# Kernel tuning notes

Measured on AMD Instinct MI355X. Metric: run time of the kernel, lower is better.

The kernel has to match this reference:

```python
import jax, jax.numpy as jnp
import numpy as np

PERIOD = 7   # statsmodels seasonal_decompose period used in season()
L_P = 16     # patch length hardcoded in patches()
STRIDE = 8   # stride hardcoded in patches()

B, C, L, D = 16, 64, 512, 768


def _decompose(x):
    """Vectorized additive seasonal_decompose (period=7) over last axis.

    Matches statsmodels: trend = centered 7-pt moving average (edges NaN in
    statsmodels; represented as 0 here so the math stays finite), seasonal =
    de-meaned per-phase average of the detrended interior, resid = x - trend
    - seasonal on the valid interior (0 at edges, where statsmodels has NaN).
    x: [B, C, L]
    """
    Lx = x.shape[-1]
    half = PERIOD // 2  # 3
    cs = jnp.concatenate([jnp.zeros(x.shape[:-1] + (1,), x.dtype), jnp.cumsum(x, -1)], -1)
    ma = (cs[..., PERIOD:] - cs[..., :-PERIOD]) / PERIOD  # [B,C,L-6] centers 3..L-4
    trend = jnp.zeros_like(x).at[..., half:Lx - half].set(ma)
    idx = jnp.arange(Lx)
    mask = (idx >= half) & (idx < Lx - half)          # valid interior
    ph = idx % PERIOD
    det = jnp.where(mask, x - trend, 0.0)             # detrended (0 where invalid)
    Pm = jax.nn.one_hot(ph, PERIOD, dtype=x.dtype) * mask[:, None].astype(x.dtype)  # [L,7]
    sums = jnp.einsum('bcl,lp->bcp', det, Pm)         # per-phase sums over valid idx
    counts = Pm.sum(0)                                # per-phase valid counts
    pavg = sums / counts
    pavg = pavg - pavg.mean(-1, keepdims=True)        # de-mean the 7 phase averages
    seasonal = jnp.take(pavg, ph, axis=-1)            # tile to [B,C,L]
    resid = jnp.where(mask, x - trend - seasonal, 0.0)
    return trend, seasonal, resid


def setup_inputs() -> dict:
    key = jax.random.key(0)
    ks = jax.random.split(key, 12)
    s = 0.02
    return {
        'data_x': jax.random.normal(ks[0], (B, C, L), jnp.float32),
        'data_y': jax.random.normal(ks[1], (B, C, L), jnp.float32),
        'gamma': jax.random.uniform(ks[2], (B, C, L), jnp.float32),
        'beta': jax.random.uniform(ks[3], (B, C, L), jnp.float32),
        'w_trend': jax.random.normal(ks[4], (L_P, L), jnp.float32) * s,
        'b_trend': jax.random.normal(ks[5], (L_P,), jnp.float32) * s,
        'w_seasonal': jax.random.normal(ks[6], (L_P, L), jnp.float32) * s,
        'b_seasonal': jax.random.normal(ks[7], (L_P,), jnp.float32) * s,
        'w_resid': jax.random.normal(ks[8], (L_P, L), jnp.float32) * s,
        'b_resid': jax.random.normal(ks[9], (L_P,), jnp.float32) * s,
        'w_g': jax.random.normal(ks[10], (D, 3 * L_P), jnp.float32) * s,
        'b_g': jax.random.normal(ks[11], (D,), jnp.float32) * s,
    }


def reference(data_x, data_y, gamma, beta, w_trend, b_trend, w_seasonal,
              b_seasonal, w_resid, b_resid, w_g, b_g):
    Lx = data_x.shape[-1]
    # transformed(): RevIN-like affine with mean/sqrt(var) (epsi=0, unbiased var)
    mean = data_x.mean(1)
    var = data_x.var(1, ddof=1)
    m = (mean / jnp.sqrt(var))[:, None, :]
    xt = gamma * (data_x - m) + beta
    # season() detaches its input in the original
    xt = jax.lax.stop_gradient(xt)
    trend, seasonal, resid = _decompose(xt)
    # patches(): per-stream Linear(L->16), concat, Linear(48->D)
    t = trend @ w_trend.T + b_trend          # [B,C,16]
    s = seasonal @ w_seasonal.T + b_seasonal
    r = resid @ w_resid.T + b_resid
    cat = jnp.concatenate([t, s, r], -1)     # [B,C,48]
    p = cat @ w_g.T + b_g                    # [B,C,D]
    # unsqueeze(2).expand(...) before cat -> every patch slot is identical
    N_p = int((Lx + L_P) / STRIDE + 2)
    return jnp.broadcast_to(p[:, :, None, :], p.shape[:2] + (N_p, p.shape[-1]))
```

## Files before the change

### kernel.cpp

```cpp
#include <hip/hip_runtime.h>

#define Bx 16
#define Cx 64
#define Lx 512
#define Dx 768
#define NPx 68
#define PER 7

__global__ void mean_var_kernel(const float* __restrict__ x,
                                float* __restrict__ m) {
    int idx = blockIdx.x * blockDim.x + threadIdx.x;
    if (idx >= Bx * Lx) return;
    int b = idx / Lx, l = idx - b * Lx;
    const float* xp = x + (size_t)b * Cx * Lx + l;
    float s = 0.f, ss = 0.f;
#pragma unroll 8
    for (int c = 0; c < Cx; ++c) {
        float v = xp[(size_t)c * Lx];
        s += v;
        ss += v * v;
    }
    float mean = s / (float)Cx;
    float var = (ss - s * s / (float)Cx) / (float)(Cx - 1);
    m[idx] = mean * rsqrtf(var);
}

__global__ __launch_bounds__(256) void token_kernel(
    const float* __restrict__ x, const float* __restrict__ gamma,
    const float* __restrict__ beta, const float* __restrict__ m,
    const float* __restrict__ w_t, const float* __restrict__ b_t,
    const float* __restrict__ w_s, const float* __restrict__ b_s,
    const float* __restrict__ w_r, const float* __restrict__ b_r,
    const float* __restrict__ w_g, const float* __restrict__ b_g,
    float* __restrict__ out) {
    __shared__ __align__(16) float s_xt[Lx];
    __shared__ __align__(16) float s_tr[Lx];
    __shared__ __align__(16) float s_se[Lx];
    __shared__ __align__(16) float s_res[Lx];
    __shared__ float s_ph[PER];
    __shared__ __align__(16) float s_cat[48];

    const int bc = blockIdx.x;
    const int b = bc / Cx;
    const int tid = threadIdx.x;

    const float* xp = x + (size_t)bc * Lx;
    const float* gp = gamma + (size_t)bc * Lx;
    const float* bp = beta + (size_t)bc * Lx;
    const float* mp = m + (size_t)b * Lx;

    for (int l = tid; l < Lx; l += 256)
        s_xt[l] = gp[l] * (xp[l] - mp[l]) + bp[l];
    __syncthreads();

    for (int l = tid; l < Lx; l += 256) {
        float t = 0.f;
        if (l >= 3 && l <= Lx - 4) {
#pragma unroll
            for (int k = -3; k <= 3; ++k) t += s_xt[l + k];
            t *= (1.f / 7.f);
        }
        s_tr[l] = t;
    }
    __syncthreads();

    if (tid < PER) {
        int p = tid;
        int l0 = p + 7 * ((3 - p + 6) / 7);
        float sum = 0.f;
        int cnt = 0;
        for (int l = l0; l <= Lx - 4; l += 7) {
            sum += s_xt[l] - s_tr[l];
            ++cnt;
        }
        s_ph[p] = sum / (float)cnt;
    }
    __syncthreads();
    if (tid == 0) {
        float mn = 0.f;
#pragma unroll
        for (int p = 0; p < PER; ++p) mn += s_ph[p];
        mn *= (1.f / 7.f);
#pragma unroll
        for (int p = 0; p < PER; ++p) s_ph[p] -= mn;
    }
    __syncthreads();

    for (int l = tid; l < Lx; l += 256) {
        float se = s_ph[l % PER];
        s_se[l] = se;
        s_res[l] = (l >= 3 && l <= Lx - 4) ? (s_xt[l] - s_tr[l] - se) : 0.f;
    }
    __syncthreads();

    {
        int j = tid >> 2, q = tid & 3;
        if (j < 48) {
            const float* stream;
            const float* w;
            const float* bias;
            int jj;
            if (j < 16) {
                stream = s_tr; w = w_t; bias = b_t; jj = j;
            } else if (j < 32) {
                stream = s_se; w = w_s; bias = b_s; jj = j - 16;
            } else {
                stream = s_res; w = w_r; bias = b_r; jj = j - 32;
            }
            const float4* wr =
                reinterpret_cast<const float4*>(w + (size_t)jj * Lx + q * 128);
            const float4* sp = reinterpret_cast<const float4*>(stream + q * 128);
            float acc = 0.f;
#pragma unroll
            for (int i = 0; i < 32; ++i) {
                float4 a = sp[i], wv = wr[i];
                acc += a.x * wv.x + a.y * wv.y + a.z * wv.z + a.w * wv.w;
            }
            acc += __shfl_xor(acc, 1);
            acc += __shfl_xor(acc, 2);
            if (q == 0) s_cat[j] = acc + bias[jj];
        }
    }
    __syncthreads();

    float* outp = out + (size_t)bc * NPx * Dx;
    const float4* c4 = reinterpret_cast<const float4*>(s_cat);
    for (int d = tid; d < Dx; d += 256) {
        const float4* wg4 = reinterpret_cast<const float4*>(w_g + (size_t)d * 48);
        float acc = 0.f;
#pragma unroll
        for (int kk = 0; kk < 12; ++kk) {
            float4 w4 = wg4[kk], cc = c4[kk];
            acc += w4.x * cc.x + w4.y * cc.y + w4.z * cc.z + w4.w * cc.w;
        }
        outp[d] = acc + b_g[d];
    }
}

__global__ __launch_bounds__(256) void broadcast_kernel(float* __restrict__ out) {
    int gid = blockIdx.x * 256 + threadIdx.x;
    int d4 = gid % 192;
    int tmp = gid / 192;
    int bc = tmp & 1023;
    int chunk = tmp >> 10;

    float4* row = reinterpret_cast<float4*>(out) + (size_t)bc * (NPx * 192);
    float4 v = row[d4];

    int n0 = 1 + chunk * 17;
    int cnt = min(17, NPx - n0);
    float4* dst = row + (size_t)n0 * 192 + d4;
    for (int n = 0; n < cnt; ++n) dst[n * 192] = v;
}

extern "C" void kernel_launch(void* const* d_in, const int* in_sizes, int n_in,
                              void* d_out, int out_size, void* d_ws,
                              size_t ws_size, hipStream_t stream) {
    const float* data_x = (const float*)d_in[0];
    const float* gamma = (const float*)d_in[2];
    const float* beta = (const float*)d_in[3];
    const float* w_t = (const float*)d_in[4];
    const float* b_t = (const float*)d_in[5];
    const float* w_s = (const float*)d_in[6];
    const float* b_s = (const float*)d_in[7];
    const float* w_r = (const float*)d_in[8];
    const float* b_r = (const float*)d_in[9];
    const float* w_g = (const float*)d_in[10];
    const float* b_g = (const float*)d_in[11];
    float* out = (float*)d_out;
    float* m = (float*)d_ws;

    int nthreads_m = Bx * Lx;
    mean_var_kernel<<<(nthreads_m + 255) / 256, 256, 0, stream>>>(data_x, m);

    token_kernel<<<Bx * Cx, 256, 0, stream>>>(data_x, gamma, beta, m, w_t, b_t,
                                              w_s, b_s, w_r, b_r, w_g, b_g,
                                              out);

    broadcast_kernel<<<(4 * Bx * Cx * 192) / 256, 256, 0, stream>>>(out);
}
```

Before: 69.75 us.

## Fuse mean/var, token compute and broadcast into one kernel

Merges the three kernels into a single per-(b,c) block. Each block recomputes the channel mean/variance for its batch (redundantly, 64 blocks per batch read the same 128KB slice) and writes all 68 patch copies directly from shared memory. The phase-average reduction is also parallelized across warps with shuffles. This removes two launches and the read-back of the first row in the broadcast pass, at the cost of redundant reads of data_x per block.

```diff
diff --git a/kernel.cpp b/kernel.cpp
--- a/kernel.cpp
+++ b/kernel.cpp
@@ -7,73 +7,98 @@
 #define NPx 68
 #define PER 7
 
-__global__ void mean_var_kernel(const float* __restrict__ x,
-                                float* __restrict__ m) {
-    int idx = blockIdx.x * blockDim.x + threadIdx.x;
-    if (idx >= Bx * Lx) return;
-    int b = idx / Lx, l = idx - b * Lx;
-    const float* xp = x + (size_t)b * Cx * Lx + l;
-    float s = 0.f, ss = 0.f;
-#pragma unroll 8
-    for (int c = 0; c < Cx; ++c) {
-        float v = xp[(size_t)c * Lx];
-        s += v;
-        ss += v * v;
-    }
-    float mean = s / (float)Cx;
-    float var = (ss - s * s / (float)Cx) / (float)(Cx - 1);
-    m[idx] = mean * rsqrtf(var);
-}
-
-__global__ __launch_bounds__(256) void token_kernel(
+__global__ __launch_bounds__(256) void fused_kernel(
     const float* __restrict__ x, const float* __restrict__ gamma,
-    const float* __restrict__ beta, const float* __restrict__ m,
+    const float* __restrict__ beta,
     const float* __restrict__ w_t, const float* __restrict__ b_t,
     const float* __restrict__ w_s, const float* __restrict__ b_s,
     const float* __restrict__ w_r, const float* __restrict__ b_r,
     const float* __restrict__ w_g, const float* __restrict__ b_g,
     float* __restrict__ out) {
+    __shared__ __align__(16) float s_m[Lx];
     __shared__ __align__(16) float s_xt[Lx];
     __shared__ __align__(16) float s_tr[Lx];
+    __shared__ __align__(16) float s_det[Lx];
     __shared__ __align__(16) float s_se[Lx];
     __shared__ __align__(16) float s_res[Lx];
     __shared__ float s_ph[PER];
     __shared__ __align__(16) float s_cat[48];
+    __shared__ __align__(16) float s_p[Dx];
+    __shared__ __align__(16) float red_s[2][128][4];
+    __shared__ __align__(16) float red_ss[2][128][4];
 
     const int bc = blockIdx.x;
-    const int b = bc / Cx;
+    const int b = bc >> 6;
     const int tid = threadIdx.x;
 
-    const float* xp = x + (size_t)bc * Lx;
-    const float* gp = gamma + (size_t)bc * Lx;
-    const float* bp = beta + (size_t)bc * Lx;
-    const float* mp = m + (size_t)b * Lx;
+    const float* xrow = x + (size_t)bc * Lx;
+    const float* grow = gamma + (size_t)bc * Lx;
+    const float* brow = beta + (size_t)bc * Lx;
+    float xv0 = xrow[tid], xv1 = xrow[tid + 256];
+    float gv0 = grow[tid], gv1 = grow[tid + 256];
+    float bv0 = brow[tid], bv1 = brow[tid + 256];
 
-    for (int l = tid; l < Lx; l += 256)
-        s_xt[l] = gp[l] * (xp[l] - mp[l]) + bp[l];
+    {
+        int g = tid >> 7, j = tid & 127;
+        const float* xb = x + (size_t)b * Cx * Lx + (size_t)g * 32 * Lx + 4 * j;
+        float s0 = 0.f, s1 = 0.f, s2 = 0.f, s3 = 0.f;
+        float q0 = 0.f, q1 = 0.f, q2 = 0.f, q3 = 0.f;
+#pragma unroll 4
+        for (int c = 0; c < 32; ++c) {
+            float4 v = *reinterpret_cast<const float4*>(xb + (size_t)c * Lx);
+            s0 += v.x; s1 += v.y; s2 += v.z; s3 += v.w;
+            q0 += v.x * v.x; q1 += v.y * v.y; q2 += v.z * v.z; q3 += v.w * v.w;
+        }
+        red_s[g][j][0] = s0; red_s[g][j][1] = s1;
+        red_s[g][j][2] = s2; red_s[g][j][3] = s3;
+        red_ss[g][j][0] = q0; red_ss[g][j][1] = q1;
+        red_ss[g][j][2] = q2; red_ss[g][j][3] = q3;
+    }
+    __syncthreads();
+    if (tid < 128) {
+#pragma unroll
+        for (int k = 0; k < 4; ++k) {
+            float s = red_s[0][tid][k] + red_s[1][tid][k];
+            float q = red_ss[0][tid][k] + red_ss[1][tid][k];
+            float mean = s * (1.f / (float)Cx);
+            float var = (q - s * s * (1.f / (float)Cx)) * (1.f / (float)(Cx - 1));
+            s_m[4 * tid + k] = mean * rsqrtf(var);
+        }
+    }
     __syncthreads();
 
-    for (int l = tid; l < Lx; l += 256) {
-        float t = 0.f;
+    s_xt[tid] = gv0 * (xv0 - s_m[tid]) + bv0;
+    s_xt[tid + 256] = gv1 * (xv1 - s_m[tid + 256]) + bv1;
+    __syncthreads();
+
+#pragma unroll
+    for (int u = 0; u < 2; ++u) {
+        int l = tid + u * 256;
+        float t = 0.f, d = 0.f;
         if (l >= 3 && l <= Lx - 4) {
 #pragma unroll
             for (int k = -3; k <= 3; ++k) t += s_xt[l + k];
             t *= (1.f / 7.f);
+            d = s_xt[l] - t;
         }
         s_tr[l] = t;
+        s_det[l] = d;
     }
     __syncthreads();
 
-    if (tid < PER) {
-        int p = tid;
+    if (tid < 224) {
+        int p = tid >> 5, j = tid & 31;
         int l0 = p + 7 * ((3 - p + 6) / 7);
+        int cnt = (Lx - 4 - l0) / 7 + 1;
         float sum = 0.f;
-        int cnt = 0;
-        for (int l = l0; l <= Lx - 4; l += 7) {
-            sum += s_xt[l] - s_tr[l];
-            ++cnt;
+#pragma unroll
+        for (int k = 0; k < 3; ++k) {
+            int idx = j + 32 * k;
+            if (idx < cnt) sum += s_det[l0 + 7 * idx];
         }
-        s_ph[p] = sum / (float)cnt;
+#pragma unroll
+        for (int off = 16; off >= 1; off >>= 1) sum += __shfl_xor(sum, off);
+        if (j == 0) s_ph[p] = sum / (float)cnt;
     }
     __syncthreads();
     if (tid == 0) {
@@ -86,71 +111,67 @@
     }
     __syncthreads();
 
-    for (int l = tid; l < Lx; l += 256) {
+#pragma unroll
+    for (int u = 0; u < 2; ++u) {
+        int l = tid + u * 256;
         float se = s_ph[l % PER];
         s_se[l] = se;
-        s_res[l] = (l >= 3 && l <= Lx - 4) ? (s_xt[l] - s_tr[l] - se) : 0.f;
+        s_res[l] = (l >= 3 && l <= Lx - 4) ? (s_det[l] - se) : 0.f;
+    }
+    __syncthreads();
+
+    if (tid < 192) {
+        int j = tid >> 2, q = tid & 3;
+        const float* stream;
+        const float* w;
+        const float* bias;
+        int jj;
+        if (j < 16) {
+            stream = s_tr; w = w_t; bias = b_t; jj = j;
+        } else if (j < 32) {
+            stream = s_se; w = w_s; bias = b_s; jj = j - 16;
+        } else {
+            stream = s_res; w = w_r; bias = b_r; jj = j - 32;
+        }
+        const float4* wr =
+            reinterpret_cast<const float4*>(w + (size_t)jj * Lx + q * 128);
+        const float4* sp = reinterpret_cast<const float4*>(stream + q * 128);
+        float acc = 0.f;
+#pragma unroll 8
+        for (int i = 0; i < 32; ++i) {
+            float4 a = sp[i], wv = wr[i];
+            acc += a.x * wv.x + a.y * wv.y + a.z * wv.z + a.w * wv.w;
+        }
+        acc += __shfl_xor(acc, 1);
+        acc += __shfl_xor(acc, 2);
+        if (q == 0) s_cat[j] = acc + bias[jj];
     }
     __syncthreads();
 
     {
-        int j = tid >> 2, q = tid & 3;
-        if (j < 48) {
-            const float* stream;
-            const float* w;
-            const float* bias;
-            int jj;
-            if (j < 16) {
-                stream = s_tr; w = w_t; bias = b_t; jj = j;
-            } else if (j < 32) {
-                stream = s_se; w = w_s; bias = b_s; jj = j - 16;
-            } else {
-                stream = s_res; w = w_r; bias = b_r; jj = j - 32;
-            }
-            const float4* wr =
-                reinterpret_cast<const float4*>(w + (size_t)jj * Lx + q * 128);
-            const float4* sp = reinterpret_cast<const float4*>(stream + q * 128);
+        const float4* c4 = reinterpret_cast<const float4*>(s_cat);
+#pragma unroll
+        for (int u = 0; u < 3; ++u) {
+            int d = tid + u * 256;
+            const float4* wg4 =
+                reinterpret_cast<const float4*>(w_g + (size_t)d * 48);
             float acc = 0.f;
 #pragma unroll
-            for (int i = 0; i < 32; ++i) {
-                float4 a = sp[i], wv = wr[i];
-                acc += a.x * wv.x + a.y * wv.y + a.z * wv.z + a.w * wv.w;
+            for (int kk = 0; kk < 12; ++kk) {
+                float4 w4 = wg4[kk], cc = c4[kk];
+                acc += w4.x * cc.x + w4.y * cc.y + w4.z * cc.z + w4.w * cc.w;
             }
-            acc += __shfl_xor(acc, 1);
-            acc += __shfl_xor(acc, 2);
-            if (q == 0) s_cat[j] = acc + bias[jj];
+            s_p[d] = acc + b_g[d];
         }
     }
     __syncthreads();
 
-    float* outp = out + (size_t)bc * NPx * Dx;
-    const float4* c4 = reinterpret_cast<const float4*>(s_cat);
-    for (int d = tid; d < Dx; d += 256) {
-        const float4* wg4 = reinterpret_cast<const float4*>(w_g + (size_t)d * 48);
-        float acc = 0.f;
+    if (tid < 192) {
+        float4 v = reinterpret_cast<const float4*>(s_p)[tid];
+        float4* dst = reinterpret_cast<float4*>(out + (size_t)bc * NPx * Dx) + tid;
 #pragma unroll
-        for (int kk = 0; kk < 12; ++kk) {
-            float4 w4 = wg4[kk], cc = c4[kk];
-            acc += w4.x * cc.x + w4.y * cc.y + w4.z * cc.z + w4.w * cc.w;
-        }
-        outp[d] = acc + b_g[d];
+        for (int n = 0; n < NPx; ++n) dst[(size_t)n * 192] = v;
     }
-}
-
-__global__ __launch_bounds__(256) void broadcast_kernel(float* __restrict__ out) {
-    int gid = blockIdx.x * 256 + threadIdx.x;
-    int d4 = gid % 192;
-    int tmp = gid / 192;
-    int bc = tmp & 1023;
-    int chunk = tmp >> 10;
-
-    float4* row = reinterpret_cast<float4*>(out) + (size_t)bc * (NPx * 192);
-    float4 v = row[d4];
-
-    int n0 = 1 + chunk * 17;
-    int cnt = min(17, NPx - n0);
-    float4* dst = row + (size_t)n0 * 192 + d4;
-    for (int n = 0; n < cnt; ++n) dst[n * 192] = v;
 }
 
 extern "C" void kernel_launch(void* const* d_in, const int* in_sizes, int n_in,
@@ -168,14 +189,8 @@
     const float* w_g = (const float*)d_in[10];
     const float* b_g = (const float*)d_in[11];
     float* out = (float*)d_out;
-    float* m = (float*)d_ws;
 
-    int nthreads_m = Bx * Lx;
-    mean_var_kernel<<<(nthreads_m + 255) / 256, 256, 0, stream>>>(data_x, m);
-
-    token_kernel<<<Bx * Cx, 256, 0, stream>>>(data_x, gamma, beta, m, w_t, b_t,
+    fused_kernel<<<Bx * Cx, 256, 0, stream>>>(data_x, gamma, beta, w_t, b_t,
                                               w_s, b_s, w_r, b_r, w_g, b_g,
                                               out);
-
-    broadcast_kernel<<<(4 * Bx * Cx * 192) / 256, 256, 0, stream>>>(out);
 }
```

Result: faster. 68.15 us (-2.3%).

## Write compact projection to workspace and expand with grid-stride streaming kernel

Applied to the files above, without the earlier changes.

The token kernel now writes the [B,C,D] projection to a compact workspace buffer instead of slot 0 of the output. A new grid-stride expand kernel then writes every output slot as a contiguous linear stream, replacing the old broadcast kernel that read slot 0 and wrote strided chunks. Separately, the per-phase seasonal averages are computed with 224 threads and wave shuffles over a precomputed detrended array instead of 7 serial threads, and the fixed-trip loops are unrolled. The main cost being attacked is the output write pattern; the change adds a small extra workspace round trip.

```diff
diff --git a/kernel.cpp b/kernel.cpp
--- a/kernel.cpp
+++ b/kernel.cpp
@@ -6,6 +6,8 @@
 #define Dx 768
 #define NPx 68
 #define PER 7
+#define TOT4 (Bx * Cx * NPx * (Dx / 4))
+#define ROW4 (NPx * (Dx / 4))
 
 __global__ void mean_var_kernel(const float* __restrict__ x,
                                 float* __restrict__ m) {
@@ -32,16 +34,17 @@
     const float* __restrict__ w_s, const float* __restrict__ b_s,
     const float* __restrict__ w_r, const float* __restrict__ b_r,
     const float* __restrict__ w_g, const float* __restrict__ b_g,
-    float* __restrict__ out) {
+    float* __restrict__ p) {
     __shared__ __align__(16) float s_xt[Lx];
     __shared__ __align__(16) float s_tr[Lx];
+    __shared__ __align__(16) float s_det[Lx];
     __shared__ __align__(16) float s_se[Lx];
     __shared__ __align__(16) float s_res[Lx];
     __shared__ float s_ph[PER];
     __shared__ __align__(16) float s_cat[48];
 
     const int bc = blockIdx.x;
-    const int b = bc / Cx;
+    const int b = bc >> 6;
     const int tid = threadIdx.x;
 
     const float* xp = x + (size_t)bc * Lx;
@@ -49,108 +52,118 @@
     const float* bp = beta + (size_t)bc * Lx;
     const float* mp = m + (size_t)b * Lx;
 
-    for (int l = tid; l < Lx; l += 256)
+#pragma unroll
+    for (int u = 0; u < 2; ++u) {
+        int l = tid + u * 256;
         s_xt[l] = gp[l] * (xp[l] - mp[l]) + bp[l];
+    }
     __syncthreads();
 
-    for (int l = tid; l < Lx; l += 256) {
-        float t = 0.f;
+#pragma unroll
+    for (int u = 0; u < 2; ++u) {
+        int l = tid + u * 256;
+        float t = 0.f, d = 0.f;
         if (l >= 3 && l <= Lx - 4) {
 #pragma unroll
             for (int k = -3; k <= 3; ++k) t += s_xt[l + k];
             t *= (1.f / 7.f);
+            d = s_xt[l] - t;
         }
         s_tr[l] = t;
+        s_det[l] = d;
     }
     __syncthreads();
 
-    if (tid < PER) {
-        int p = tid;
-        int l0 = p + 7 * ((3 - p + 6) / 7);
+    if (tid < 224) {
+        int ph = tid >> 5, j = tid & 31;
+        int l0 = ph + 7 * ((3 - ph + 6) / 7);
+        int cnt = (Lx - 4 - l0) / 7 + 1;
         float sum = 0.f;
-        int cnt = 0;
-        for (int l = l0; l <= Lx - 4; l += 7) {
-            sum += s_xt[l] - s_tr[l];
-            ++cnt;
+#pragma unroll
+        for (int k = 0; k < 3; ++k) {
+            int idx = j + 32 * k;
+            if (idx < cnt) sum += s_det[l0 + 7 * idx];
         }
-        s_ph[p] = sum / (float)cnt;
+#pragma unroll
+        for (int off = 16; off >= 1; off >>= 1) sum += __shfl_xor(sum, off);
+        if (j == 0) s_ph[ph] = sum / (float)cnt;
     }
     __syncthreads();
     if (tid == 0) {
         float mn = 0.f;
 #pragma unroll
-        for (int p = 0; p < PER; ++p) mn += s_ph[p];
+        for (int q = 0; q < PER; ++q) mn += s_ph[q];
         mn *= (1.f / 7.f);
 #pragma unroll
-        for (int p = 0; p < PER; ++p) s_ph[p] -= mn;
+        for (int q = 0; q < PER; ++q) s_ph[q] -= mn;
     }
     __syncthreads();
 
-    for (int l = tid; l < Lx; l += 256) {
+#pragma unroll
+    for (int u = 0; u < 2; ++u) {
+        int l = tid + u * 256;
         float se = s_ph[l % PER];
         s_se[l] = se;
-        s_res[l] = (l >= 3 && l <= Lx - 4) ? (s_xt[l] - s_tr[l] - se) : 0.f;
+        s_res[l] = (l >= 3 && l <= Lx - 4) ? (s_det[l] - se) : 0.f;
+    }
+    __syncthreads();
+
+    if (tid < 192) {
+        int j = tid >> 2, q = tid & 3;
+        const float* stream;
+        const float* w;
+        const float* bias;
+        int jj;
+        if (j < 16) {
+            stream = s_tr; w = w_t; bias = b_t; jj = j;
+        } else if (j < 32) {
+            stream = s_se; w = w_s; bias = b_s; jj = j - 16;
+        } else {
+            stream = s_res; w = w_r; bias = b_r; jj = j - 32;
+        }
+        const float4* wr =
+            reinterpret_cast<const float4*>(w + (size_t)jj * Lx + q * 128);
+        const float4* sp = reinterpret_cast<const float4*>(stream + q * 128);
+        float acc = 0.f;
+#pragma unroll 8
+        for (int i = 0; i < 32; ++i) {
+            float4 a = sp[i], wv = wr[i];
+            acc += a.x * wv.x + a.y * wv.y + a.z * wv.z + a.w * wv.w;
+        }
+        acc += __shfl_xor(acc, 1);
+        acc += __shfl_xor(acc, 2);
+        if (q == 0) s_cat[j] = acc + bias[jj];
     }
     __syncthreads();
 
     {
-        int j = tid >> 2, q = tid & 3;
-        if (j < 48) {
-            const float* stream;
-            const float* w;
-            const float* bias;
-            int jj;
-            if (j < 16) {
-                stream = s_tr; w = w_t; bias = b_t; jj = j;
-            } else if (j < 32) {
-                stream = s_se; w = w_s; bias = b_s; jj = j - 16;
-            } else {
-                stream = s_res; w = w_r; bias = b_r; jj = j - 32;
-            }
-            const float4* wr =
-                reinterpret_cast<const float4*>(w + (size_t)jj * Lx + q * 128);
-            const float4* sp = reinterpret_cast<const float4*>(stream + q * 128);
+        const float4* c4 = reinterpret_cast<const float4*>(s_cat);
+        float* prow = p + (size_t)bc * Dx;
+#pragma unroll
+        for (int u = 0; u < 3; ++u) {
+            int d = tid + u * 256;
+            const float4* wg4 =
+                reinterpret_cast<const float4*>(w_g + (size_t)d * 48);
             float acc = 0.f;
 #pragma unroll
-            for (int i = 0; i < 32; ++i) {
-                float4 a = sp[i], wv = wr[i];
-                acc += a.x * wv.x + a.y * wv.y + a.z * wv.z + a.w * wv.w;
+            for (int kk = 0; kk < 12; ++kk) {
+                float4 w4 = wg4[kk], cc = c4[kk];
+                acc += w4.x * cc.x + w4.y * cc.y + w4.z * cc.z + w4.w * cc.w;
             }
-            acc += __shfl_xor(acc, 1);
-            acc += __shfl_xor(acc, 2);
-            if (q == 0) s_cat[j] = acc + bias[jj];
+            prow[d] = acc + b_g[d];
         }
-    }
-    __syncthreads();
-
-    float* outp = out + (size_t)bc * NPx * Dx;
-    const float4* c4 = reinterpret_cast<const float4*>(s_cat);
-    for (int d = tid; d < Dx; d += 256) {
-        const float4* wg4 = reinterpret_cast<const float4*>(w_g + (size_t)d * 48);
-        float acc = 0.f;
-#pragma unroll
-        for (int kk = 0; kk < 12; ++kk) {
-            float4 w4 = wg4[kk], cc = c4[kk];
-            acc += w4.x * cc.x + w4.y * cc.y + w4.z * cc.z + w4.w * cc.w;
-        }
-        outp[d] = acc + b_g[d];
     }
 }
 
-__global__ __launch_bounds__(256) void broadcast_kernel(float* __restrict__ out) {
-    int gid = blockIdx.x * 256 + threadIdx.x;
-    int d4 = gid % 192;
-    int tmp = gid / 192;
-    int bc = tmp & 1023;
-    int chunk = tmp >> 10;
-
-    float4* row = reinterpret_cast<float4*>(out) + (size_t)bc * (NPx * 192);
-    float4 v = row[d4];
-
-    int n0 = 1 + chunk * 17;
-    int cnt = min(17, NPx - n0);
-    float4* dst = row + (size_t)n0 * 192 + d4;
-    for (int n = 0; n < cnt; ++n) dst[n * 192] = v;
+__global__ __launch_bounds__(256) void expand_kernel(
+    const float4* __restrict__ p4, float4* __restrict__ out4) {
+    int stride = gridDim.x * 256;
+    for (int i4 = blockIdx.x * 256 + threadIdx.x; i4 < TOT4; i4 += stride) {
+        int bc = (int)((unsigned)i4 / (unsigned)ROW4);
+        int r = i4 - bc * ROW4;
+        int d4 = (int)((unsigned)r % 192u);
+        out4[i4] = p4[bc * 192 + d4];
+    }
 }
 
 extern "C" void kernel_launch(void* const* d_in, const int* in_sizes, int n_in,
@@ -168,14 +181,15 @@
     const float* w_g = (const float*)d_in[10];
     const float* b_g = (const float*)d_in[11];
     float* out = (float*)d_out;
+
     float* m = (float*)d_ws;
+    float* p = (float*)d_ws + Bx * Lx;
 
-    int nthreads_m = Bx * Lx;
-    mean_var_kernel<<<(nthreads_m + 255) / 256, 256, 0, stream>>>(data_x, m);
+    mean_var_kernel<<<(Bx * Lx + 255) / 256, 256, 0, stream>>>(data_x, m);
 
     token_kernel<<<Bx * Cx, 256, 0, stream>>>(data_x, gamma, beta, m, w_t, b_t,
-                                              w_s, b_s, w_r, b_r, w_g, b_g,
-                                              out);
+                                              w_s, b_s, w_r, b_r, w_g, b_g, p);
 
-    broadcast_kernel<<<(4 * Bx * Cx * 192) / 256, 256, 0, stream>>>(out);
+    expand_kernel<<<4096, 256, 0, stream>>>(
+        reinterpret_cast<const float4*>(p), reinterpret_cast<float4*>(out));
 }
```

Result: slower. 86.98 us (+24.7%).

## Fuse broadcast into token kernel with two blocks per row writing halves

Applied to the files above, without the earlier changes.

Drops the separate broadcast kernel. Each (b,c) row is now handled by two blocks, and each block redundantly computes the decomposition and projections, keeps the projected vector in shared memory, then writes its half of the 68 broadcast copies. This removes the global read-back of the first row and one kernel launch. In exchange, the per-row compute is duplicated across the two blocks.

```diff
diff --git a/kernel.cpp b/kernel.cpp
--- a/kernel.cpp
+++ b/kernel.cpp
@@ -6,6 +6,8 @@
 #define Dx 768
 #define NPx 68
 #define PER 7
+#define ROW4 (NPx * (Dx / 4))
+#define HALF4 (ROW4 / 2)
 
 __global__ void mean_var_kernel(const float* __restrict__ x,
                                 float* __restrict__ m) {
@@ -39,9 +41,11 @@
     __shared__ __align__(16) float s_res[Lx];
     __shared__ float s_ph[PER];
     __shared__ __align__(16) float s_cat[48];
+    __shared__ __align__(16) float s_p[Dx];
 
-    const int bc = blockIdx.x;
-    const int b = bc / Cx;
+    const int bc = blockIdx.x >> 1;
+    const int h = blockIdx.x & 1;
+    const int b = bc >> 6;
     const int tid = threadIdx.x;
 
     const float* xp = x + (size_t)bc * Lx;
@@ -123,34 +127,27 @@
     }
     __syncthreads();
 
-    float* outp = out + (size_t)bc * NPx * Dx;
-    const float4* c4 = reinterpret_cast<const float4*>(s_cat);
     for (int d = tid; d < Dx; d += 256) {
         const float4* wg4 = reinterpret_cast<const float4*>(w_g + (size_t)d * 48);
+        const float4* c4 = reinterpret_cast<const float4*>(s_cat);
         float acc = 0.f;
 #pragma unroll
         for (int kk = 0; kk < 12; ++kk) {
             float4 w4 = wg4[kk], cc = c4[kk];
             acc += w4.x * cc.x + w4.y * cc.y + w4.z * cc.z + w4.w * cc.w;
         }
-        outp[d] = acc + b_g[d];
+        s_p[d] = acc + b_g[d];
     }
-}
+    __syncthreads();
 
-__global__ __launch_bounds__(256) void broadcast_kernel(float* __restrict__ out) {
-    int gid = blockIdx.x * 256 + threadIdx.x;
-    int d4 = gid % 192;
-    int tmp = gid / 192;
-    int bc = tmp & 1023;
-    int chunk = tmp >> 10;
-
-    float4* row = reinterpret_cast<float4*>(out) + (size_t)bc * (NPx * 192);
-    float4 v = row[d4];
-
-    int n0 = 1 + chunk * 17;
-    int cnt = min(17, NPx - n0);
-    float4* dst = row + (size_t)n0 * 192 + d4;
-    for (int n = 0; n < cnt; ++n) dst[n * 192] = v;
+    {
+        float4* outp = reinterpret_cast<float4*>(out + (size_t)bc * NPx * Dx) +
+                       (size_t)h * HALF4;
+        const float4* p4 = reinterpret_cast<const float4*>(s_p);
+        for (int i = tid; i < HALF4; i += 256) {
+            outp[i] = p4[i % 192];
+        }
+    }
 }
 
 extern "C" void kernel_launch(void* const* d_in, const int* in_sizes, int n_in,
@@ -173,9 +170,7 @@
     int nthreads_m = Bx * Lx;
     mean_var_kernel<<<(nthreads_m + 255) / 256, 256, 0, stream>>>(data_x, m);
 
-    token_kernel<<<Bx * Cx, 256, 0, stream>>>(data_x, gamma, beta, m, w_t, b_t,
-                                              w_s, b_s, w_r, b_r, w_g, b_g,
-                                              out);
-
-    broadcast_kernel<<<(4 * Bx * Cx * 192) / 256, 256, 0, stream>>>(out);
+    token_kernel<<<2 * Bx * Cx, 256, 0, stream>>>(data_x, gamma, beta, m, w_t,
+                                                  b_t, w_s, b_s, w_r, b_r, w_g,
+                                                  b_g, out);
 }
```

After: 77.62 us. +11.3%, slower.
